# Optimization experiments

Measured on AMD Instinct MI355X. Metric: run time of the kernel, lower is better.

The kernel has to match this reference:

```python
import jax, jax.numpy as jnp
import numpy as np

GAMMA = 0.99

def _get_D(gamma, T, dtype=jnp.float32):
    # D[n, m] = gamma**(n-m) if n >= m else 0 (NaN/inf cleanup as in torch source)
    n = jnp.arange(T)
    diff = n[:, None] - n[None, :]
    return jnp.where(diff >= 0, jnp.power(jnp.asarray(gamma, dtype), jnp.maximum(diff, 0).astype(dtype)), jnp.zeros((), dtype))

def setup_inputs() -> dict:
    key = jax.random.key(0)
    kX, kQ, kK, kV = jax.random.split(key, 4)
    B, T, I, C = 2, 4096, 1024, 1024
    X = jax.random.normal(kX, (B, T, I), dtype=jnp.float32)
    att_mask = jnp.ones((B, T), dtype=jnp.float32)
    S_n = jnp.zeros((B, C, C), dtype=jnp.float32)
    # params initialized as randn/I per the torch module
    W_Q = jax.random.normal(kQ, (I, C), dtype=jnp.float32) / I
    W_K = jax.random.normal(kK, (I, C), dtype=jnp.float32) / I
    W_V = jax.random.normal(kV, (I, I), dtype=jnp.float32) / I
    return {"X": X, "att_mask": att_mask, "S_n": S_n, "W_Q": W_Q, "W_K": W_K, "W_V": W_V}

def reference(X, att_mask, S_n, W_Q, W_K, W_V):
    # COINBlock.forward_parallel (dropout in eval mode = identity; att_mask unused)
    B, T, _ = X.shape
    C = W_Q.shape[1]
    Q = X @ W_Q            # [B,T,C]
    K = X @ W_K            # [B,T,C]
    V = X @ W_V            # [B,T,I]
    A = jnp.einsum('btc,bsc->bts', Q, K)          # [B,T,T]
    A = A * _get_D(GAMMA, T, X.dtype)[None, :, :]  # decay-masked scores
    out = A @ V                                    # [B,T,I]
    out = jnp.swapaxes(out, -2, -1).reshape(B, T, C)  # faithful transpose+view (I == C)
    return out, S_n
```

## Files before the change

### kernel.cpp

```cpp
#include <hip/hip_runtime.h>
#include <cstdint>
#include <cstddef>


using bf16x8 = __attribute__((ext_vector_type(8))) short;
using s16x4  = __attribute__((ext_vector_type(4))) short;
using f32x4  = __attribute__((ext_vector_type(4))) float;

#define T_SEQ 4096
#define C_DIM 1024

static constexpr float L2G = -0.0144995697f;

__device__ __forceinline__ short f2bf(float f) {
  unsigned u = __builtin_bit_cast(unsigned, f);
  u += 0x7FFFu + ((u >> 16) & 1u);
  return (short)(u >> 16);
}

__device__ __forceinline__ void async_ld16(const short* g, const short* l) {
  __builtin_amdgcn_global_load_lds(
      (const __attribute__((address_space(1))) unsigned int*)(uintptr_t)g,
      (__attribute__((address_space(3))) unsigned int*)(unsigned)(uintptr_t)l,
      16, 0, 0);
}

#define DSREAD(D, P) \
  asm volatile("ds_read_b128 %0, %1" : "=v"(D) : "v"((unsigned)(uintptr_t)(P)))

template<int NU>
__device__ __forceinline__ void stage_units4(const short* __restrict__ g, int ldk,
                                             short* __restrict__ l,
                                             int wave, int lane) {
  const int rl0 = lane >> 3;
  const int cu  = ((lane & 7) ^ rl0) * 8;
#pragma unroll
  for (int u = 0; u < NU; ++u)
#pragma unroll
    for (int j = 0; j < 2; ++j) {
      const int c = wave + j * 4;
      async_ld16(g + (size_t)(u * 64 + c * 8 + rl0) * ldk + cu,
                 l + u * 4096 + c * 512 + lane * 8);
    }
}

template<int NB>
__device__ __forceinline__ void gemm4w(
    const short* __restrict__ A, const short* __restrict__ B,
    int lda, int ldb, int NT,
    short* __restrict__ lsA, short* __restrict__ lsB,
    f32x4 (&acc)[4][NB])
{
  constexpr int NUB   = NB / 2;
  constexpr int BSLOT = NUB * 4096;
  const int tid  = threadIdx.x;
  const int lane = tid & 63;
  const int wave = tid >> 6;
  const int wM   = wave >> 1;
  const int wN   = wave & 1;
  const int quad = lane >> 4;
  const int l15  = lane & 15;
  const int key  = l15 & 7;
  const int uk0  = (quad ^ key) * 8;
  const int uk1  = ((4 + quad) ^ key) * 8;
  const short* aB = lsA + (wM * 64 + l15) * 64;
  const short* bB = lsB + (wN * (NB * 16) + l15) * 64;

  stage_units4<2>(A,        lda, lsA,         wave, lane);
  stage_units4<NUB>(B,      ldb, lsB,         wave, lane);
  stage_units4<2>(A + 64,   lda, lsA + 8192,  wave, lane);
  stage_units4<NUB>(B + 64, ldb, lsB + BSLOT, wave, lane);
  if constexpr (NB == 4) asm volatile("s_waitcnt vmcnt(8)" ::: "memory");
  else                   asm volatile("s_waitcnt vmcnt(6)" ::: "memory");
  __builtin_amdgcn_s_barrier();

  int sB = 0;
  for (int t = 0; t < NT; ++t) {
    const short* aS = aB + (t & 1) * 8192;
    const short* bS = bB + sB * BSLOT;
    bf16x8 af[4][2], bf[NUB][2];

#pragma unroll
    for (int i = 0; i < 4; ++i) {
      DSREAD(af[i][0], aS + i * 1024 + uk0);
      DSREAD(af[i][1], aS + i * 1024 + uk1);
    }
#pragma unroll
    for (int n = 0; n < NUB; ++n) {
      DSREAD(bf[n][0], bS + n * 1024 + uk0);
      DSREAD(bf[n][1], bS + n * 1024 + uk1);
    }
    __builtin_amdgcn_s_barrier();
    asm volatile("s_waitcnt lgkmcnt(0)" ::: "memory");
    __builtin_amdgcn_sched_barrier(0);
    __builtin_amdgcn_s_setprio(1);
#pragma unroll
    for (int kk = 0; kk < 2; ++kk)
#pragma unroll
      for (int i = 0; i < 4; ++i)
#pragma unroll
        for (int n = 0; n < NUB; ++n)
          acc[i][n] = __builtin_amdgcn_mfma_f32_16x16x32_bf16(
              af[i][kk], bf[n][kk], acc[i][n], 0, 0, 0);
    __builtin_amdgcn_s_setprio(0);
    __builtin_amdgcn_s_barrier();

#pragma unroll
    for (int n = 0; n < NUB; ++n) {
      DSREAD(bf[n][0], bS + (NUB + n) * 1024 + uk0);
      DSREAD(bf[n][1], bS + (NUB + n) * 1024 + uk1);
    }
    const bool pf = (t + 2 < NT);
    if (pf) {
      stage_units4<2>(A + (size_t)(t + 2) * 64, lda,
                      lsA + (t & 1) * 8192, wave, lane);
      int s2 = sB - 1; if (s2 < 0) s2 = 2;
      stage_units4<NUB>(B + (size_t)(t + 2) * 64, ldb,
                        lsB + s2 * BSLOT, wave, lane);
    }
    __builtin_amdgcn_s_barrier();
    asm volatile("s_waitcnt lgkmcnt(0)" ::: "memory");
    __builtin_amdgcn_sched_barrier(0);
    __builtin_amdgcn_s_setprio(1);
#pragma unroll
    for (int kk = 0; kk < 2; ++kk)
#pragma unroll
      for (int i = 0; i < 4; ++i)
#pragma unroll
        for (int n = 0; n < NUB; ++n)
          acc[i][NUB + n] = __builtin_amdgcn_mfma_f32_16x16x32_bf16(
              af[i][kk], bf[n][kk], acc[i][NUB + n], 0, 0, 0);
    __builtin_amdgcn_s_setprio(0);
    if constexpr (NB == 4) {
      if (pf) asm volatile("s_waitcnt vmcnt(8)" ::: "memory");
      else    asm volatile("s_waitcnt vmcnt(0)" ::: "memory");
    } else {
      if (pf) asm volatile("s_waitcnt vmcnt(6)" ::: "memory");
      else    asm volatile("s_waitcnt vmcnt(0)" ::: "memory");
    }
    __builtin_amdgcn_s_barrier();
    if (++sB == 3) sB = 0;
  }
}


__global__ __launch_bounds__(256) void k_convX(const float* __restrict__ x,
                                               short* __restrict__ y) {
  const size_t i = ((size_t)blockIdx.x * 256 + threadIdx.x) * 4;
  const float4 v = *(const float4*)(x + i);
  s16x4 o;
  o[0] = f2bf(v.x); o[1] = f2bf(v.y); o[2] = f2bf(v.z); o[3] = f2bf(v.w);
  *(s16x4*)(y + i) = o;
}

__global__ __launch_bounds__(256) void k_convWt(const float* __restrict__ Wq,
                                                const float* __restrict__ Wk,
                                                const float* __restrict__ Wv,
                                                short* __restrict__ Wtq,
                                                short* __restrict__ Wtk,
                                                short* __restrict__ Wtv) {
  const float* W = (blockIdx.z == 0) ? Wq : (blockIdx.z == 1) ? Wk : Wv;
  short* Wt      = (blockIdx.z == 0) ? Wtq : (blockIdx.z == 1) ? Wtk : Wtv;
  __shared__ float t[32][33];
  const int tx = threadIdx.x & 31;
  const int ty = threadIdx.x >> 5;
  const int bc = blockIdx.x * 32;
  const int bi = blockIdx.y * 32;
#pragma unroll
  for (int j = 0; j < 32; j += 8)
    t[ty + j][tx] = W[(size_t)(bi + ty + j) * 1024 + bc + tx];
  __syncthreads();
#pragma unroll
  for (int j = 0; j < 32; j += 8)
    Wt[(size_t)(bc + ty + j) * 1024 + bi + tx] = f2bf(t[tx][ty + j]);
}


__global__ __launch_bounds__(256, 2) void k_proj(
    const short* __restrict__ Xb, const short* __restrict__ Wtq,
    const short* __restrict__ Wtk, const short* __restrict__ Wtv,
    short* __restrict__ Qb, short* __restrict__ Kb, short* __restrict__ Vt) {
  __shared__ short lsA[2 * 8192];
  __shared__ short lsB[3 * 2 * 4096];
  f32x4 acc[4][4];
#pragma unroll
  for (int i = 0; i < 4; ++i)
#pragma unroll
    for (int j = 0; j < 4; ++j) acc[i][j] = 0.f;

  const int z  = blockIdx.y;
  const int bx = blockIdx.x;
  const short* Ab;
  const short* Bb;
  int m, n;
  if (z < 2) {
    m = bx >> 3; n = bx & 7;
    Ab = Xb + (size_t)m * 128 * 1024;
    Bb = (z ? Wtk : Wtq) + (size_t)n * 128 * 1024;
  } else {
    m = bx >> 6; n = bx & 63;
    Ab = Wtv + (size_t)m * 128 * 1024;
    Bb = Xb + (size_t)n * 128 * 1024;
  }
  gemm4w<4>(Ab, Bb, 1024, 1024, 16, lsA, lsB, acc);

  const int lane = threadIdx.x & 63, wave = threadIdx.x >> 6;
  const int wM = wave >> 1, wN = wave & 1;
  const int quad = lane >> 4, l15 = lane & 15;
  if (z < 2) {
    short* O = z ? Kb : Qb;
#pragma unroll
    for (int mi = 0; mi < 4; ++mi)
#pragma unroll
      for (int ni = 0; ni < 4; ++ni)
#pragma unroll
        for (int r = 0; r < 4; ++r) {
          const int row = m * 128 + wM * 64 + mi * 16 + quad * 4 + r;
          const int col = n * 128 + wN * 64 + ni * 16 + l15;
          O[(size_t)row * 1024 + col] = f2bf(acc[mi][ni][r]);
        }
  } else {
#pragma unroll
    for (int mi = 0; mi < 4; ++mi)
#pragma unroll
      for (int ni = 0; ni < 4; ++ni)
#pragma unroll
        for (int r = 0; r < 4; ++r) {
          const int crow = m * 128 + wM * 64 + mi * 16 + quad * 4 + r;
          const int t8   = n * 128 + wN * 64 + ni * 16 + l15;
          const int b = t8 >> 12, tt = t8 & 4095;
          Vt[(size_t)b * C_DIM * T_SEQ + (size_t)crow * T_SEQ + tt] =
              f2bf(acc[mi][ni][r]);
        }
  }
}

__global__ __launch_bounds__(256, 2) void k_scores(const short* __restrict__ Qb,
                                                   const short* __restrict__ Kb,
                                                   short* __restrict__ P) {
  __shared__ short lsA[2 * 8192];
  __shared__ short lsB[3 * 2 * 4096];
  f32x4 acc[4][4];
#pragma unroll
  for (int i = 0; i < 4; ++i)
#pragma unroll
    for (int j = 0; j < 4; ++j) acc[i][j] = 0.f;

  int id = blockIdx.x, mm = 0;
  while (id >= 32 - mm) { id -= 32 - mm; ++mm; }
  const int nn = mm + id;

  const size_t b = blockIdx.y;
  const short* Ab = Qb + b * T_SEQ * C_DIM + (size_t)nn * 128 * 1024;
  const short* Bb = Kb + b * T_SEQ * C_DIM + (size_t)mm * 128 * 1024;
  gemm4w<4>(Ab, Bb, 1024, 1024, 16, lsA, lsB, acc);

  short* Pb = P + b * (size_t)T_SEQ * T_SEQ;
  const int lane = threadIdx.x & 63, wave = threadIdx.x >> 6;
  const int wM = wave >> 1, wN = wave & 1;
  const int quad = lane >> 4, l15 = lane & 15;
#pragma unroll
  for (int mi = 0; mi < 4; ++mi)
#pragma unroll
    for (int ni = 0; ni < 4; ++ni)
#pragma unroll
      for (int r = 0; r < 4; ++r) {
        const int n = nn * 128 + wM * 64 + mi * 16 + quad * 4 + r;
        const int m = mm * 128 + wN * 64 + ni * 16 + l15;
        float v = 0.f;
        if (n >= m) v = acc[mi][ni][r] * exp2f((float)(n - m) * L2G);
        Pb[(size_t)n * T_SEQ + m] = f2bf(v);
      }
}

__global__ __launch_bounds__(256, 2) void k_pv(const short* __restrict__ Vt,
                                               const short* __restrict__ P,
                                               float* __restrict__ out) {
  __shared__ short lsA[2 * 8192];
  __shared__ short lsB[3 * 4096];
  const int p  = blockIdx.x;
  const int iy = blockIdx.y;
  const size_t b = blockIdx.z;

  const short* Ab = Vt + b * (size_t)C_DIM * T_SEQ + (size_t)iy * 128 * T_SEQ;
  const short* Pb = P + b * (size_t)T_SEQ * T_SEQ;
  float* Ob = out + b * (size_t)C_DIM * T_SEQ;

  const int lane = threadIdx.x & 63, wave = threadIdx.x >> 6;
  const int wM = wave >> 1, wN = wave & 1;
  const int quad = lane >> 4, l15 = lane & 15;

  const int cols[2] = { 63 - p, p };
#pragma unroll
  for (int cc = 0; cc < 2; ++cc) {
    const int c = cols[cc];
    f32x4 acc[4][2];
#pragma unroll
    for (int i = 0; i < 4; ++i) { acc[i][0] = 0.f; acc[i][1] = 0.f; }
    gemm4w<2>(Ab, Pb + (size_t)c * 64 * T_SEQ, T_SEQ, T_SEQ, c + 1, lsA, lsB, acc);
#pragma unroll
    for (int mi = 0; mi < 4; ++mi)
#pragma unroll
      for (int ni = 0; ni < 2; ++ni)
#pragma unroll
        for (int r = 0; r < 4; ++r) {
          const int irow = iy * 128 + wM * 64 + mi * 16 + quad * 4 + r;
          const int tcol = c * 64 + wN * 32 + ni * 16 + l15;
          Ob[(size_t)irow * T_SEQ + tcol] = acc[mi][ni][r];
        }
  }
}


extern "C" void kernel_launch(void* const* d_in, const int* in_sizes, int n_in,
                              void* d_out, int out_size, void* d_ws, size_t ws_size,
                              hipStream_t stream) {
  const float* X  = (const float*)d_in[0];
  const float* Wq = (const float*)d_in[3];
  const float* Wk = (const float*)d_in[4];
  const float* Wv = (const float*)d_in[5];
  float* out = (float*)d_out;

  char* ws = (char*)d_ws;
  short* Xb  = (short*)(ws);
  short* Wtq = (short*)(ws + 16777216);
  short* Wtk = (short*)(ws + 18874368);
  short* Wtv = (short*)(ws + 20971520);
  short* Qb  = (short*)(ws + 23068672);
  short* Kb  = (short*)(ws + 39845888);
  short* Vt  = (short*)(ws + 56623104);
  short* P   = (short*)(ws + 73400320);

  const size_t mainN = (size_t)2 * T_SEQ * C_DIM;
  hipMemsetAsync((char*)d_out + mainN * 4, 0,
                 ((size_t)out_size - mainN) * 4, stream);

  k_convX  <<<dim3(8192),       dim3(256), 0, stream>>>(X, Xb);
  k_convWt <<<dim3(32, 32, 3),  dim3(256), 0, stream>>>(Wq, Wk, Wv, Wtq, Wtk, Wtv);
  k_proj   <<<dim3(512, 3),     dim3(256), 0, stream>>>(Xb, Wtq, Wtk, Wtv, Qb, Kb, Vt);
  k_scores <<<dim3(528, 2),     dim3(256), 0, stream>>>(Qb, Kb, P);
  k_pv     <<<dim3(32, 8, 2),   dim3(256), 0, stream>>>(Vt, P, out);
}
```

Before: 286.6 us.

## Use 256x256 tile 8-wave GEMM for projections and precompute staging pointers

The projection kernel moves from 128x128 tiles with 4 waves to 256x256 tiles with 8 waves, using a new gemm8w routine with a double-buffered, split-phase LDS pipeline. This is meant to raise data reuse per tile and cut global traffic. In gemm4w, the inline-asm ds_read calls are replaced with plain vector loads plus compiler fences, and the global staging pointers are precomputed. The cost is fewer blocks (384) for 256 CUs, which leaves some CUs idle and adds tail imbalance, plus heavier register use from 32 accumulators per lane.

```diff
diff --git a/kernel.cpp b/kernel.cpp
--- a/kernel.cpp
+++ b/kernel.cpp
@@ -25,23 +25,130 @@
       16, 0, 0);
 }
 
-#define DSREAD(D, P) \
-  asm volatile("ds_read_b128 %0, %1" : "=v"(D) : "v"((unsigned)(uintptr_t)(P)))
-
-template<int NU>
-__device__ __forceinline__ void stage_units4(const short* __restrict__ g, int ldk,
-                                             short* __restrict__ l,
-                                             int wave, int lane) {
+#define FENCE asm volatile("" ::: "memory")
+
+__device__ __forceinline__ void gemm8w(
+    const short* __restrict__ A, const short* __restrict__ B,
+    int lda, int ldb, int NT,
+    short* __restrict__ lsA, short* __restrict__ lsB,
+    f32x4 (&acc)[8][4])
+{
+  const int tid  = threadIdx.x;
+  const int lane = tid & 63;
+  const int wave = tid >> 6;
+  const int wM   = wave >> 2;
+  const int wN   = wave & 3;
+  const int quad = lane >> 4;
+  const int l15  = lane & 15;
+  const int key  = l15 & 7;
+  const int uk0  = (quad ^ key) * 8;
+  const int uk1  = ((4 ^ quad) ^ key) * 8;
+  const short* aB0 = lsA + wM * 8192 + l15 * 64 + uk0;
+  const short* aB1 = lsA + wM * 8192 + l15 * 64 + uk1;
+  const short* bB0 = lsB + wN * 4096 + l15 * 64 + uk0;
+  const short* bB1 = lsB + wN * 4096 + l15 * 64 + uk1;
   const int rl0 = lane >> 3;
   const int cu  = ((lane & 7) ^ rl0) * 8;
-#pragma unroll
-  for (int u = 0; u < NU; ++u)
-#pragma unroll
-    for (int j = 0; j < 2; ++j) {
-      const int c = wave + j * 4;
-      async_ld16(g + (size_t)(u * 64 + c * 8 + rl0) * ldk + cu,
-                 l + u * 4096 + c * 512 + lane * 8);
-    }
+  const short* pa[4];
+  const short* pb[4];
+#pragma unroll
+  for (int j = 0; j < 4; ++j) {
+    const int grow = (wave * 4 + j) * 8 + rl0;
+    pa[j] = A + (size_t)grow * lda + cu;
+    pb[j] = B + (size_t)grow * ldb + cu;
+  }
+
+#define ST_A8(SLOT, TT)                                                             \
+  { _Pragma("unroll")                                                               \
+    for (int j = 0; j < 4; ++j)                                                     \
+      async_ld16(pa[j] + (size_t)(TT) * 64,                                         \
+                 lsA + (SLOT) * 16384 + (wave * 4 + j) * 512 + lane * 8); }
+#define ST_B8(SLOT, TT)                                                             \
+  { _Pragma("unroll")                                                               \
+    for (int j = 0; j < 4; ++j)                                                     \
+      async_ld16(pb[j] + (size_t)(TT) * 64,                                         \
+                 lsB + (SLOT) * 16384 + (wave * 4 + j) * 512 + lane * 8); }
+
+  ST_A8(0, 0);
+  ST_B8(0, 0);
+  ST_B8(1, 1);
+  asm volatile("s_waitcnt vmcnt(4)" ::: "memory");
+  __builtin_amdgcn_s_barrier();
+  FENCE;
+
+  for (int t = 0; t < NT; ++t) {
+    const int sA = (t & 1) * 16384;
+    const int sB = (t & 1) * 16384;
+    bf16x8 af[4], bf0[4], bf1[4];
+
+#pragma unroll
+    for (int mi = 0; mi < 4; ++mi)
+      af[mi] = *(const bf16x8*)(aB0 + sA + mi * 1024);
+#pragma unroll
+    for (int ni = 0; ni < 4; ++ni)
+      bf0[ni] = *(const bf16x8*)(bB0 + sB + ni * 1024);
+    if (t + 1 < NT) ST_A8((t + 1) & 1, t + 1);
+    FENCE; __builtin_amdgcn_s_barrier(); FENCE;
+    __builtin_amdgcn_s_setprio(1);
+#pragma unroll
+    for (int mi = 0; mi < 4; ++mi)
+#pragma unroll
+      for (int ni = 0; ni < 4; ++ni)
+        acc[mi][ni] = __builtin_amdgcn_mfma_f32_16x16x32_bf16(
+            af[mi], bf0[ni], acc[mi][ni], 0, 0, 0);
+    __builtin_amdgcn_s_setprio(0);
+    FENCE; __builtin_amdgcn_s_barrier(); FENCE;
+
+#pragma unroll
+    for (int mi = 0; mi < 4; ++mi)
+      af[mi] = *(const bf16x8*)(aB1 + sA + mi * 1024);
+#pragma unroll
+    for (int ni = 0; ni < 4; ++ni)
+      bf1[ni] = *(const bf16x8*)(bB1 + sB + ni * 1024);
+    FENCE; __builtin_amdgcn_s_barrier(); FENCE;
+    __builtin_amdgcn_s_setprio(1);
+#pragma unroll
+    for (int mi = 0; mi < 4; ++mi)
+#pragma unroll
+      for (int ni = 0; ni < 4; ++ni)
+        acc[mi][ni] = __builtin_amdgcn_mfma_f32_16x16x32_bf16(
+            af[mi], bf1[ni], acc[mi][ni], 0, 0, 0);
+    __builtin_amdgcn_s_setprio(0);
+    FENCE; __builtin_amdgcn_s_barrier(); FENCE;
+
+#pragma unroll
+    for (int mi = 0; mi < 4; ++mi)
+      af[mi] = *(const bf16x8*)(aB0 + sA + 4096 + mi * 1024);
+    if (t + 2 < NT) ST_B8(t & 1, t + 2);
+    FENCE; __builtin_amdgcn_s_barrier(); FENCE;
+    __builtin_amdgcn_s_setprio(1);
+#pragma unroll
+    for (int mi = 0; mi < 4; ++mi)
+#pragma unroll
+      for (int ni = 0; ni < 4; ++ni)
+        acc[4 + mi][ni] = __builtin_amdgcn_mfma_f32_16x16x32_bf16(
+            af[mi], bf0[ni], acc[4 + mi][ni], 0, 0, 0);
+    __builtin_amdgcn_s_setprio(0);
+    FENCE; __builtin_amdgcn_s_barrier(); FENCE;
+
+#pragma unroll
+    for (int mi = 0; mi < 4; ++mi)
+      af[mi] = *(const bf16x8*)(aB1 + sA + 4096 + mi * 1024);
+    FENCE; __builtin_amdgcn_s_barrier(); FENCE;
+    __builtin_amdgcn_s_setprio(1);
+#pragma unroll
+    for (int mi = 0; mi < 4; ++mi)
+#pragma unroll
+      for (int ni = 0; ni < 4; ++ni)
+        acc[4 + mi][ni] = __builtin_amdgcn_mfma_f32_16x16x32_bf16(
+            af[mi], bf1[ni], acc[4 + mi][ni], 0, 0, 0);
+    __builtin_amdgcn_s_setprio(0);
+    if (t + 2 < NT) asm volatile("s_waitcnt vmcnt(4)" ::: "memory");
+    else            asm volatile("s_waitcnt vmcnt(0)" ::: "memory");
+    FENCE; __builtin_amdgcn_s_barrier(); FENCE;
+  }
+#undef ST_A8
+#undef ST_B8
 }
 
 template<int NB>
@@ -66,13 +173,42 @@
   const short* aB = lsA + (wM * 64 + l15) * 64;
   const short* bB = lsB + (wN * (NB * 16) + l15) * 64;
 
-  stage_units4<2>(A,        lda, lsA,         wave, lane);
-  stage_units4<NUB>(B,      ldb, lsB,         wave, lane);
-  stage_units4<2>(A + 64,   lda, lsA + 8192,  wave, lane);
-  stage_units4<NUB>(B + 64, ldb, lsB + BSLOT, wave, lane);
+  const int rl0 = lane >> 3;
+  const int cu  = ((lane & 7) ^ rl0) * 8;
+  const short* pa4[2][2];
+  const short* pb4[NUB][2];
+#pragma unroll
+  for (int u = 0; u < 2; ++u)
+#pragma unroll
+    for (int j = 0; j < 2; ++j)
+      pa4[u][j] = A + (size_t)(u * 64 + (wave + 4 * j) * 8 + rl0) * lda + cu;
+#pragma unroll
+  for (int u = 0; u < NUB; ++u)
+#pragma unroll
+    for (int j = 0; j < 2; ++j)
+      pb4[u][j] = B + (size_t)(u * 64 + (wave + 4 * j) * 8 + rl0) * ldb + cu;
+
+#define ST_A4(SLOT, TT)                                                             \
+  { _Pragma("unroll")                                                               \
+    for (int u = 0; u < 2; ++u)                                                     \
+      _Pragma("unroll")                                                             \
+      for (int j = 0; j < 2; ++j)                                                   \
+        async_ld16(pa4[u][j] + (size_t)(TT) * 64,                                   \
+                   lsA + (SLOT) * 8192 + u * 4096 + (wave + 4 * j) * 512 + lane * 8); }
+#define ST_B4(SLOT, TT)                                                             \
+  { _Pragma("unroll")                                                               \
+    for (int u = 0; u < NUB; ++u)                                                   \
+      _Pragma("unroll")                                                             \
+      for (int j = 0; j < 2; ++j)                                                   \
+        async_ld16(pb4[u][j] + (size_t)(TT) * 64,                                   \
+                   lsB + (SLOT) * BSLOT + u * 4096 + (wave + 4 * j) * 512 + lane * 8); }
+
+  ST_A4(0, 0); ST_B4(0, 0);
+  ST_A4(1, 1); ST_B4(1, 1);
   if constexpr (NB == 4) asm volatile("s_waitcnt vmcnt(8)" ::: "memory");
   else                   asm volatile("s_waitcnt vmcnt(6)" ::: "memory");
   __builtin_amdgcn_s_barrier();
+  FENCE;
 
   int sB = 0;
   for (int t = 0; t < NT; ++t) {
@@ -82,17 +218,15 @@
 
 #pragma unroll
     for (int i = 0; i < 4; ++i) {
-      DSREAD(af[i][0], aS + i * 1024 + uk0);
-      DSREAD(af[i][1], aS + i * 1024 + uk1);
+      af[i][0] = *(const bf16x8*)&aS[i * 1024 + uk0];
+      af[i][1] = *(const bf16x8*)&aS[i * 1024 + uk1];
     }
 #pragma unroll
     for (int n = 0; n < NUB; ++n) {
-      DSREAD(bf[n][0], bS + n * 1024 + uk0);
-      DSREAD(bf[n][1], bS + n * 1024 + uk1);
+      bf[n][0] = *(const bf16x8*)&bS[n * 1024 + uk0];
+      bf[n][1] = *(const bf16x8*)&bS[n * 1024 + uk1];
     }
-    __builtin_amdgcn_s_barrier();
-    asm volatile("s_waitcnt lgkmcnt(0)" ::: "memory");
-    __builtin_amdgcn_sched_barrier(0);
+    FENCE; __builtin_amdgcn_s_barrier(); FENCE;
     __builtin_amdgcn_s_setprio(1);
 #pragma unroll
     for (int kk = 0; kk < 2; ++kk)
@@ -103,24 +237,20 @@
           acc[i][n] = __builtin_amdgcn_mfma_f32_16x16x32_bf16(
               af[i][kk], bf[n][kk], acc[i][n], 0, 0, 0);
     __builtin_amdgcn_s_setprio(0);
-    __builtin_amdgcn_s_barrier();
+    FENCE; __builtin_amdgcn_s_barrier(); FENCE;
 
 #pragma unroll
     for (int n = 0; n < NUB; ++n) {
-      DSREAD(bf[n][0], bS + (NUB + n) * 1024 + uk0);
-      DSREAD(bf[n][1], bS + (NUB + n) * 1024 + uk1);
+      bf[n][0] = *(const bf16x8*)&bS[(NUB + n) * 1024 + uk0];
+      bf[n][1] = *(const bf16x8*)&bS[(NUB + n) * 1024 + uk1];
     }
     const bool pf = (t + 2 < NT);
     if (pf) {
-      stage_units4<2>(A + (size_t)(t + 2) * 64, lda,
-                      lsA + (t & 1) * 8192, wave, lane);
+      ST_A4(t & 1, t + 2);
       int s2 = sB - 1; if (s2 < 0) s2 = 2;
-      stage_units4<NUB>(B + (size_t)(t + 2) * 64, ldb,
-                        lsB + s2 * BSLOT, wave, lane);
+      ST_B4(s2, t + 2);
     }
-    __builtin_amdgcn_s_barrier();
-    asm volatile("s_waitcnt lgkmcnt(0)" ::: "memory");
-    __builtin_amdgcn_sched_barrier(0);
+    FENCE; __builtin_amdgcn_s_barrier(); FENCE;
     __builtin_amdgcn_s_setprio(1);
 #pragma unroll
     for (int kk = 0; kk < 2; ++kk)
@@ -138,9 +268,11 @@
       if (pf) asm volatile("s_waitcnt vmcnt(6)" ::: "memory");
       else    asm volatile("s_waitcnt vmcnt(0)" ::: "memory");
     }
-    __builtin_amdgcn_s_barrier();
+    FENCE; __builtin_amdgcn_s_barrier(); FENCE;
     if (++sB == 3) sB = 0;
   }
+#undef ST_A4
+#undef ST_B4
 }
 
 
@@ -176,15 +308,15 @@
 }
 
 
-__global__ __launch_bounds__(256, 2) void k_proj(
+__global__ __launch_bounds__(512, 1) void k_proj(
     const short* __restrict__ Xb, const short* __restrict__ Wtq,
     const short* __restrict__ Wtk, const short* __restrict__ Wtv,
     short* __restrict__ Qb, short* __restrict__ Kb, short* __restrict__ Vt) {
-  __shared__ short lsA[2 * 8192];
-  __shared__ short lsB[3 * 2 * 4096];
-  f32x4 acc[4][4];
-#pragma unroll
-  for (int i = 0; i < 4; ++i)
+  __shared__ short lsA[2 * 16384];
+  __shared__ short lsB[2 * 16384];
+  f32x4 acc[8][4];
+#pragma unroll
+  for (int i = 0; i < 8; ++i)
 #pragma unroll
     for (int j = 0; j < 4; ++j) acc[i][j] = 0.f;
 
@@ -194,40 +326,40 @@
   const short* Bb;
   int m, n;
   if (z < 2) {
-    m = bx >> 3; n = bx & 7;
-    Ab = Xb + (size_t)m * 128 * 1024;
-    Bb = (z ? Wtk : Wtq) + (size_t)n * 128 * 1024;
+    m = bx >> 2; n = bx & 3;
+    Ab = Xb + (size_t)m * 256 * 1024;
+    Bb = (z ? Wtk : Wtq) + (size_t)n * 256 * 1024;
   } else {
-    m = bx >> 6; n = bx & 63;
-    Ab = Wtv + (size_t)m * 128 * 1024;
-    Bb = Xb + (size_t)n * 128 * 1024;
-  }
-  gemm4w<4>(Ab, Bb, 1024, 1024, 16, lsA, lsB, acc);
+    m = bx >> 5; n = bx & 31;
+    Ab = Wtv + (size_t)m * 256 * 1024;
+    Bb = Xb + (size_t)n * 256 * 1024;
+  }
+  gemm8w(Ab, Bb, 1024, 1024, 16, lsA, lsB, acc);
 
   const int lane = threadIdx.x & 63, wave = threadIdx.x >> 6;
-  const int wM = wave >> 1, wN = wave & 1;
+  const int wM = wave >> 2, wN = wave & 3;
   const int quad = lane >> 4, l15 = lane & 15;
   if (z < 2) {
     short* O = z ? Kb : Qb;
 #pragma unroll
-    for (int mi = 0; mi < 4; ++mi)
+    for (int mi = 0; mi < 8; ++mi)
 #pragma unroll
       for (int ni = 0; ni < 4; ++ni)
 #pragma unroll
         for (int r = 0; r < 4; ++r) {
-          const int row = m * 128 + wM * 64 + mi * 16 + quad * 4 + r;
-          const int col = n * 128 + wN * 64 + ni * 16 + l15;
+          const int row = m * 256 + wM * 128 + mi * 16 + quad * 4 + r;
+          const int col = n * 256 + wN * 64 + ni * 16 + l15;
           O[(size_t)row * 1024 + col] = f2bf(acc[mi][ni][r]);
         }
   } else {
 #pragma unroll
-    for (int mi = 0; mi < 4; ++mi)
+    for (int mi = 0; mi < 8; ++mi)
 #pragma unroll
       for (int ni = 0; ni < 4; ++ni)
 #pragma unroll
         for (int r = 0; r < 4; ++r) {
-          const int crow = m * 128 + wM * 64 + mi * 16 + quad * 4 + r;
-          const int t8   = n * 128 + wN * 64 + ni * 16 + l15;
+          const int crow = m * 256 + wM * 128 + mi * 16 + quad * 4 + r;
+          const int t8   = n * 256 + wN * 64 + ni * 16 + l15;
           const int b = t8 >> 12, tt = t8 & 4095;
           Vt[(size_t)b * C_DIM * T_SEQ + (size_t)crow * T_SEQ + tt] =
               f2bf(acc[mi][ni][r]);
@@ -337,7 +469,7 @@
 
   k_convX  <<<dim3(8192),       dim3(256), 0, stream>>>(X, Xb);
   k_convWt <<<dim3(32, 32, 3),  dim3(256), 0, stream>>>(Wq, Wk, Wv, Wtq, Wtk, Wtv);
-  k_proj   <<<dim3(512, 3),     dim3(256), 0, stream>>>(Xb, Wtq, Wtk, Wtv, Qb, Kb, Vt);
+  k_proj   <<<dim3(128, 3),     dim3(512), 0, stream>>>(Xb, Wtq, Wtk, Wtv, Qb, Kb, Vt);
   k_scores <<<dim3(528, 2),     dim3(256), 0, stream>>>(Qb, Kb, P);
   k_pv     <<<dim3(32, 8, 2),   dim3(256), 0, stream>>>(Vt, P, out);
 }
```

Result: faster. 280.2 us (-2.2%).
